# Kernel optimization log

Measured on AMD Instinct MI355X. Metric: run time of the kernel, lower is better.

Reference implementation:

```python
import jax, jax.numpy as jnp
import numpy as np

N_WIRES = 8
DIM = 2 ** N_WIRES  # 256


def _rx(theta):
    # theta: [] or [N] -> [2,2] or [N,2,2] complex64
    c = jnp.cos(theta / 2)
    s = jnp.sin(theta / 2)
    return jnp.stack([jnp.stack([c + 0j, -1j * s], -1),
                      jnp.stack([-1j * s, c + 0j], -1)], -2)


def _ry(theta):
    c = jnp.cos(theta / 2)
    s = jnp.sin(theta / 2)
    return jnp.stack([jnp.stack([c + 0j, -s + 0j], -1),
                      jnp.stack([s + 0j, c + 0j], -1)], -2)


def _rz(theta):
    e = jnp.exp(-1j * theta / 2)
    z = jnp.zeros_like(e)
    return jnp.stack([jnp.stack([e, z], -1),
                      jnp.stack([z, jnp.conj(e)], -1)], -2)


def _apply_1q(state, U, wire):
    # state: [N, DIM]; U: [2,2] (shared) or [N,2,2] (per-sample)
    s = state.reshape(-1, 2 ** wire, 2, 2 ** (N_WIRES - 1 - wire))
    if U.ndim == 2:
        s = jnp.einsum('ab,nxby->nxay', U, s)
    else:
        s = jnp.einsum('nab,nxby->nxay', U, s)
    return s.reshape(-1, DIM)


def _cnot(state, c, t):
    # wire 0 = most significant bit (PennyLane convention)
    s = state.reshape((-1,) + (2,) * N_WIRES)
    ax_c = 1 + c
    s0 = jnp.take(s, 0, axis=ax_c)
    s1 = jnp.take(s, 1, axis=ax_c)
    ax_t = 1 + t if t < c else t  # target axis after control axis removed
    s1 = jnp.flip(s1, axis=ax_t)
    s = jnp.stack([s0, s1], axis=ax_c)
    return s.reshape(-1, DIM)


def _z_signs():
    idx = np.arange(DIM)
    bits = (idx[:, None] >> (N_WIRES - 1 - np.arange(N_WIRES))[None, :]) & 1
    return jnp.asarray(1.0 - 2.0 * bits, dtype=jnp.float32)  # [DIM, 8]


def _circuit(x_flat, params):
    # x_flat: [N, 8] angles; params: [8, 3]
    n = x_flat.shape[0]
    state = jnp.zeros((n, DIM), dtype=jnp.complex64).at[:, 0].set(1.0)
    for i in range(N_WIRES):
        state = _apply_1q(state, _rx(x_flat[:, i]), i)
    for i in range(N_WIRES):
        state = _apply_1q(state, _ry(params[i, 0]), i)
        state = _apply_1q(state, _rz(params[i, 1]), i)
        state = _apply_1q(state, _rx(params[i, 2]), i)
    for i in range(N_WIRES - 1):
        state = _cnot(state, i, i + 1)
    state = _cnot(state, N_WIRES - 1, 0)
    probs = state.real ** 2 + state.imag ** 2  # [N, DIM]
    return probs @ _z_signs()  # [N, 8] PauliZ expvals


def setup_inputs() -> dict:
    key = jax.random.key(0)
    ks = jax.random.split(key, 4)
    B, S = 16, 2048
    embed_dim, ffn_dim = 512, 2048
    return {
        'x': jax.random.normal(ks[0], (B, S, N_WIRES), dtype=jnp.float32),
        'params': jax.random.normal(ks[1], (N_WIRES, 3), dtype=jnp.float32),
        'W1': jax.random.normal(ks[2], (ffn_dim, N_WIRES), dtype=jnp.float32) * 0.1,
        'b1': jnp.zeros((ffn_dim,), dtype=jnp.float32),
        'W2': jax.random.normal(ks[3], (embed_dim, ffn_dim), dtype=jnp.float32) * 0.02,
        'b2': jnp.zeros((embed_dim,), dtype=jnp.float32),
    }


def reference(x, params, W1, b1, W2, b2):
    B, S, _ = x.shape
    ev = _circuit(x.reshape(-1, N_WIRES), params).reshape(B, S, N_WIRES)
    h = jax.nn.relu(ev @ W1.T + b1)
    return h @ W2.T + b2
```

## Files before the change

### kernel.cpp

```cpp
#include <hip/hip_runtime.h>
#include <hip/hip_bf16.h>

#define NS 32768
#define EMB 512
#define KDIM 2048
#define BM 256
#define BN 128
#define NITER (KDIM / 32)

typedef float f32x16 __attribute__((ext_vector_type(16)));
typedef __bf16 bf16x8 __attribute__((ext_vector_type(8)));
typedef __bf16 bf16x2 __attribute__((ext_vector_type(2)));
typedef unsigned int u32;
typedef const __attribute__((address_space(1))) u32* gptr_t;
typedef __attribute__((address_space(3))) u32* lptr_t;

__device__ __forceinline__ void gload_lds16(const void* g, void* l) {
    __builtin_amdgcn_global_load_lds((gptr_t)g, (lptr_t)l, 16, 0, 0);
}

__device__ __forceinline__ u32 pkrelu(float lo, float hi) {
    union { bf16x2 h; u32 u; } c;
    c.h[0] = (__bf16)fmaxf(lo, 0.f);
    c.h[1] = (__bf16)fmaxf(hi, 0.f);
    return c.u;
}

__device__ __forceinline__ bf16x8 mk_af(u32 a, u32 b, u32 c, u32 d) {
    union { u32 u[4]; bf16x8 v; } t;
    t.u[0] = a; t.u[1] = b; t.u[2] = c; t.u[3] = d;
    return t.v;
}

__device__ __forceinline__ void h_to_af(const f32x16 h, bf16x8& af0, bf16x8& af1) {
    af0 = mk_af(pkrelu(h[0], h[1]),  pkrelu(h[2], h[3]),
                pkrelu(h[4], h[5]),  pkrelu(h[6], h[7]));
    af1 = mk_af(pkrelu(h[8], h[9]),  pkrelu(h[10], h[11]),
                pkrelu(h[12], h[13]), pkrelu(h[14], h[15]));
}

__global__ __launch_bounds__(256) void k_prep(const float* __restrict__ W2,
                                              const float* __restrict__ W1,
                                              __hip_bfloat16* __restrict__ W2b,
                                              __hip_bfloat16* __restrict__ W1bg) {
    int t = threadIdx.x;
    if (blockIdx.x < 1024) {
        int i = (blockIdx.x * 256 + t) * 4;
        float4 v = *(const float4*)(W2 + i);
        __hip_bfloat16 o[4];
        o[0] = __float2bfloat16(v.x); o[1] = __float2bfloat16(v.y);
        o[2] = __float2bfloat16(v.z); o[3] = __float2bfloat16(v.w);
        *(ulong1*)(W2b + i) = *(ulong1*)o;
    } else {
        int j = (blockIdx.x - 1024) * 1024 + t * 4;
        float4 w = *(const float4*)(W1 + j);
        __hip_bfloat16 p[4];
        p[0] = __float2bfloat16(w.x); p[1] = __float2bfloat16(w.y);
        p[2] = __float2bfloat16(w.z); p[3] = __float2bfloat16(w.w);
        *(ulong1*)(W1bg + j) = *(ulong1*)p;
    }
}

__global__ __launch_bounds__(256, 2) void k_gemm(
        const float* __restrict__ x,
        const float* __restrict__ params,
        const __hip_bfloat16* __restrict__ W1bg,
        const float* __restrict__ b1,
        const __hip_bfloat16* __restrict__ W2b,
        const float* __restrict__ b2,
        float* __restrict__ C) {
    __shared__ __hip_bfloat16 Bs[4][8 * 512];
    __shared__ __hip_bfloat16 W1s[KDIM * 8];
    __shared__ __hip_bfloat16 b1h[KDIM];
    __shared__ __hip_bfloat16 evs[BM * 8];

    int tid = threadIdx.x, wave = tid >> 6, lane = tid & 63;
    int l31 = lane & 31, half = lane >> 5;
    int bx = blockIdx.x, bm = bx >> 2, bn = bx & 3;

    {
        float K1[8], K2[8];
        #pragma unroll
        for (int i = 0; i < 8; i++) {
            float a = params[i*3+0], b = params[i*3+1], g = params[i*3+2];
            float sa, ca, sb, cb, sg, cg;
            __sincosf(a, &sa, &ca);
            __sincosf(b, &sb, &cb);
            __sincosf(g, &sg, &cg);
            K1[i] = sa*sb*sg + ca*cg;
            K2[i] = cb*sg;
        }
        int n = bm * BM + tid;
        float4 x0 = *(const float4*)(x + (size_t)n*8);
        float4 x1 = *(const float4*)(x + (size_t)n*8 + 4);
        float xs[8] = {x0.x, x0.y, x0.z, x0.w, x1.x, x1.y, x1.z, x1.w};
        float z[8];
        #pragma unroll
        for (int i = 0; i < 8; i++) {
            float s, c;
            __sincosf(xs[i], &s, &c);
            z[i] = c * K1[i] - s * K2[i];
        }
        float evv[8];
        float p = z[0];
        #pragma unroll
        for (int j = 1; j < 8; j++) { p *= z[j]; evv[j] = p; }
        float sfx = z[7];
        #pragma unroll
        for (int j = 6; j >= 1; j--) sfx *= z[j];
        evv[0] = sfx;
        __hip_bfloat16 o[8];
        #pragma unroll
        for (int i = 0; i < 8; i++) o[i] = __float2bfloat16(evv[i]);
        *(bf16x8*)&evs[tid * 8] = *(bf16x8*)o;
    }
    for (int i = tid; i < KDIM; i += 256) {
        int q = (i >> 2) & 3;
        int src = i + ((q == 1) ? 4 : (q == 2) ? -4 : 0);
        *(bf16x8*)&W1s[i * 8] = *(const bf16x8*)(W1bg + (size_t)src * 8);
        b1h[i] = __float2bfloat16(b1[src]);
    }

    const __hip_bfloat16* gBp[2];
    #pragma unroll
    for (int i = 0; i < 2; i++) {
        int f = wave * 2 + i, ni = f >> 1, t = f & 1;
        gBp[i] = W2b + (size_t)(bn*BN + ni*32 + l31) * KDIM + t*16 + half*8;
    }
    #pragma unroll
    for (int b = 0; b < 2; b++) {
        #pragma unroll
        for (int i = 0; i < 2; i++) {
            gload_lds16(gBp[i], &Bs[b][(wave*2 + i) * 512]);
            gBp[i] += 32;
        }
    }

    __syncthreads();

    bf16x8 evB0, evB1;
    if (half == 0) {
        evB0 = *(bf16x8*)&evs[(wave * 64 +      l31) * 8];
        evB1 = *(bf16x8*)&evs[(wave * 64 + 32 + l31) * 8];
    } else {
        evB0 = (bf16x8){};
        evB0[0] = (__bf16)1.0f;
        evB1 = evB0;
    }
    const f32x16 z16 = {};

    f32x16 acc[8] = {};

#define COMPUTE_AF(K0, A00, A01, A10, A11) do {                               \
        bf16x8 w1f;                                                           \
        if (half == 0) {                                                      \
            w1f = *(const bf16x8*)&W1s[((K0) + l31) * 8];                     \
        } else {                                                              \
            w1f = (bf16x8){};                                                 \
            w1f[0] = *(const __bf16*)&b1h[(K0) + l31];                        \
        }                                                                     \
        f32x16 h0 = __builtin_amdgcn_mfma_f32_32x32x16_bf16(w1f, evB0, z16, 0, 0, 0); \
        h_to_af(h0, A00, A01);                                                \
        f32x16 h1 = __builtin_amdgcn_mfma_f32_32x32x16_bf16(w1f, evB1, z16, 0, 0, 0); \
        h_to_af(h1, A10, A11);                                                \
    } while (0)

#define GEMM2_STEP(CB, A00, A01, A10, A11) do {                               \
        __builtin_amdgcn_s_setprio(1);                                        \
        _Pragma("unroll")                                                     \
        for (int ni = 0; ni < 4; ni++) {                                      \
            bf16x8 bf0 = *(bf16x8*)&Bs[CB][(ni*2 + 0) * 512 + lane * 8];      \
            acc[ni]     = __builtin_amdgcn_mfma_f32_32x32x16_bf16(A00, bf0, acc[ni],     0, 0, 0); \
            acc[4 + ni] = __builtin_amdgcn_mfma_f32_32x32x16_bf16(A10, bf0, acc[4 + ni], 0, 0, 0); \
            bf16x8 bf1 = *(bf16x8*)&Bs[CB][(ni*2 + 1) * 512 + lane * 8];      \
            acc[ni]     = __builtin_amdgcn_mfma_f32_32x32x16_bf16(A01, bf1, acc[ni],     0, 0, 0); \
            acc[4 + ni] = __builtin_amdgcn_mfma_f32_32x32x16_bf16(A11, bf1, acc[4 + ni], 0, 0, 0); \
        }                                                                     \
        __builtin_amdgcn_s_setprio(0);                                        \
    } while (0)

#define K_ITER(T, BUF, DO_STAGE, VMC) do {                                    \
        if (DO_STAGE) {                                                       \
            gload_lds16(gBp[0], &Bs[((BUF) + 2) & 3][(wave*2 + 0) * 512]);    \
            gload_lds16(gBp[1], &Bs[((BUF) + 2) & 3][(wave*2 + 1) * 512]);    \
            gBp[0] += 32; gBp[1] += 32;                                       \
        }                                                                     \
        COMPUTE_AF((T) * 32, aA00, aA01, aA10, aA11);                         \
        asm volatile("s_waitcnt vmcnt(" VMC ")" ::: "memory");                \
        __builtin_amdgcn_s_barrier();                                         \
        GEMM2_STEP(BUF, aA00, aA01, aA10, aA11);                              \
    } while (0)

    bf16x8 aA00, aA01, aA10, aA11;

    for (int it0 = 0; it0 < NITER - 4; it0 += 4) {
        K_ITER(it0 + 0, 0, 1, "4");
        K_ITER(it0 + 1, 1, 1, "4");
        K_ITER(it0 + 2, 2, 1, "4");
        K_ITER(it0 + 3, 3, 1, "4");
    }
    K_ITER(NITER - 4, 0, 1, "4");
    K_ITER(NITER - 3, 1, 1, "4");
    K_ITER(NITER - 2, 2, 0, "2");
    K_ITER(NITER - 1, 3, 0, "0");

#undef K_ITER
#undef COMPUTE_AF
#undef GEMM2_STEP

    #pragma unroll
    for (int rg = 0; rg < 2; rg++) {
        int rbase = bm*BM + wave*64 + rg*32 + 4*half;
        #pragma unroll
        for (int ni = 0; ni < 4; ni++) {
            int col = bn*BN + ni*32 + l31;
            float bias = b2[col];
            #pragma unroll
            for (int r = 0; r < 16; r++) {
                int row = rbase + (r & 3) + 8 * (r >> 2);
                C[(size_t)row * EMB + col] = acc[rg*4 + ni][r] + bias;
            }
        }
    }
}

extern "C" void kernel_launch(void* const* d_in, const int* in_sizes, int n_in,
                              void* d_out, int out_size, void* d_ws, size_t ws_size,
                              hipStream_t stream) {
    const float* x      = (const float*)d_in[0];
    const float* params = (const float*)d_in[1];
    const float* W1     = (const float*)d_in[2];
    const float* b1     = (const float*)d_in[3];
    const float* W2     = (const float*)d_in[4];
    const float* b2     = (const float*)d_in[5];
    float* out = (float*)d_out;

    char* ws = (char*)d_ws;
    __hip_bfloat16* W2b  = (__hip_bfloat16*)ws;
    __hip_bfloat16* W1bg = (__hip_bfloat16*)(ws + 2097152);

    k_prep<<<1040, 256, 0, stream>>>(W2, W1, W2b, W1bg);
    k_gemm<<<(NS/BM) * (EMB/BN), 256, 0, stream>>>(x, params, W1bg, b1, W2b, b2, out);
}
```

Baseline: 147.9 us.

## Fuse weight bf16 conversion into GEMM kernel via register-staged W2 loads

Removes the separate prep kernel that converted W2 and W1 to bf16. The GEMM kernel now loads fp32 W2 directly into registers, converts it to bf16 and writes it to LDS with a register-staged software pipeline. This replaces the async global-to-LDS loads. It saves one kernel launch and the intermediate round trip through global memory, but each block now reads twice the W2 bytes (fp32), and the conversion work is repeated by every block that shares the same W2 columns. The pipeline also changes from a 2-deep LDS prefetch to a 1-deep register prefetch, which may expose more load latency.

```diff
diff --git a/kernel.cpp b/kernel.cpp
--- a/kernel.cpp
+++ b/kernel.cpp
@@ -12,11 +12,12 @@
 typedef __bf16 bf16x8 __attribute__((ext_vector_type(8)));
 typedef __bf16 bf16x2 __attribute__((ext_vector_type(2)));
 typedef unsigned int u32;
-typedef const __attribute__((address_space(1))) u32* gptr_t;
-typedef __attribute__((address_space(3))) u32* lptr_t;
-
-__device__ __forceinline__ void gload_lds16(const void* g, void* l) {
-    __builtin_amdgcn_global_load_lds((gptr_t)g, (lptr_t)l, 16, 0, 0);
+
+__device__ __forceinline__ u32 pk2(float lo, float hi) {
+    union { bf16x2 h; u32 u; } c;
+    c.h[0] = (__bf16)lo;
+    c.h[1] = (__bf16)hi;
+    return c.u;
 }
 
 __device__ __forceinline__ u32 pkrelu(float lo, float hi) {
@@ -39,40 +40,18 @@
                 pkrelu(h[12], h[13]), pkrelu(h[14], h[15]));
 }
 
-__global__ __launch_bounds__(256) void k_prep(const float* __restrict__ W2,
-                                              const float* __restrict__ W1,
-                                              __hip_bfloat16* __restrict__ W2b,
-                                              __hip_bfloat16* __restrict__ W1bg) {
-    int t = threadIdx.x;
-    if (blockIdx.x < 1024) {
-        int i = (blockIdx.x * 256 + t) * 4;
-        float4 v = *(const float4*)(W2 + i);
-        __hip_bfloat16 o[4];
-        o[0] = __float2bfloat16(v.x); o[1] = __float2bfloat16(v.y);
-        o[2] = __float2bfloat16(v.z); o[3] = __float2bfloat16(v.w);
-        *(ulong1*)(W2b + i) = *(ulong1*)o;
-    } else {
-        int j = (blockIdx.x - 1024) * 1024 + t * 4;
-        float4 w = *(const float4*)(W1 + j);
-        __hip_bfloat16 p[4];
-        p[0] = __float2bfloat16(w.x); p[1] = __float2bfloat16(w.y);
-        p[2] = __float2bfloat16(w.z); p[3] = __float2bfloat16(w.w);
-        *(ulong1*)(W1bg + j) = *(ulong1*)p;
-    }
-}
-
 __global__ __launch_bounds__(256, 2) void k_gemm(
         const float* __restrict__ x,
         const float* __restrict__ params,
-        const __hip_bfloat16* __restrict__ W1bg,
+        const float* __restrict__ W1,
         const float* __restrict__ b1,
-        const __hip_bfloat16* __restrict__ W2b,
+        const float* __restrict__ W2,
         const float* __restrict__ b2,
         float* __restrict__ C) {
-    __shared__ __hip_bfloat16 Bs[4][8 * 512];
-    __shared__ __hip_bfloat16 W1s[KDIM * 8];
-    __shared__ __hip_bfloat16 b1h[KDIM];
-    __shared__ __hip_bfloat16 evs[BM * 8];
+    __shared__ __align__(16) __hip_bfloat16 Bs[4][8 * 512];
+    __shared__ __align__(16) __hip_bfloat16 W1s[KDIM * 8];
+    __shared__ __align__(16) __hip_bfloat16 b1h[KDIM];
+    __shared__ __align__(16) __hip_bfloat16 evs[BM * 8];
 
     int tid = threadIdx.x, wave = tid >> 6, lane = tid & 63;
     int l31 = lane & 31, half = lane >> 5;
@@ -117,25 +96,44 @@
     for (int i = tid; i < KDIM; i += 256) {
         int q = (i >> 2) & 3;
         int src = i + ((q == 1) ? 4 : (q == 2) ? -4 : 0);
-        *(bf16x8*)&W1s[i * 8] = *(const bf16x8*)(W1bg + (size_t)src * 8);
+        float4 wa = *(const float4*)(W1 + (size_t)src * 8);
+        float4 wb = *(const float4*)(W1 + (size_t)src * 8 + 4);
+        union { u32 u[4]; bf16x8 v; } cw;
+        cw.u[0] = pk2(wa.x, wa.y); cw.u[1] = pk2(wa.z, wa.w);
+        cw.u[2] = pk2(wb.x, wb.y); cw.u[3] = pk2(wb.z, wb.w);
+        *(bf16x8*)&W1s[i * 8] = cw.v;
         b1h[i] = __float2bfloat16(b1[src]);
     }
 
-    const __hip_bfloat16* gBp[2];
-    #pragma unroll
-    for (int i = 0; i < 2; i++) {
-        int f = wave * 2 + i, ni = f >> 1, t = f & 1;
-        gBp[i] = W2b + (size_t)(bn*BN + ni*32 + l31) * KDIM + t*16 + half*8;
-    }
-    #pragma unroll
-    for (int b = 0; b < 2; b++) {
-        #pragma unroll
-        for (int i = 0; i < 2; i++) {
-            gload_lds16(gBp[i], &Bs[b][(wave*2 + i) * 512]);
-            gBp[i] += 32;
-        }
-    }
-
+    const float* gW0;
+    const float* gW1;
+    {
+        int f0 = wave * 2 + 0, f1 = wave * 2 + 1;
+        gW0 = W2 + (size_t)(bn*BN + (f0 >> 1)*32 + l31) * KDIM + (f0 & 1)*16 + half*8;
+        gW1 = W2 + (size_t)(bn*BN + (f1 >> 1)*32 + l31) * KDIM + (f1 & 1)*16 + half*8;
+    }
+    float4 rA0, rA1, rB0, rB1;
+
+#define LOADW2() do {                                                         \
+        rA0 = *(const float4*)gW0; rA1 = *(const float4*)(gW0 + 4);           \
+        rB0 = *(const float4*)gW1; rB1 = *(const float4*)(gW1 + 4);           \
+        gW0 += 32; gW1 += 32;                                                 \
+    } while (0)
+
+#define CVTWRITE(BUFIDX) do {                                                 \
+        union { u32 u[4]; bf16x8 v; } c0, c1;                                 \
+        c0.u[0] = pk2(rA0.x, rA0.y); c0.u[1] = pk2(rA0.z, rA0.w);             \
+        c0.u[2] = pk2(rA1.x, rA1.y); c0.u[3] = pk2(rA1.z, rA1.w);             \
+        c1.u[0] = pk2(rB0.x, rB0.y); c1.u[1] = pk2(rB0.z, rB0.w);             \
+        c1.u[2] = pk2(rB1.x, rB1.y); c1.u[3] = pk2(rB1.z, rB1.w);             \
+        *(bf16x8*)&Bs[BUFIDX][(wave*2 + 0) * 512 + lane * 8] = c0.v;          \
+        *(bf16x8*)&Bs[BUFIDX][(wave*2 + 1) * 512 + lane * 8] = c1.v;          \
+    } while (0)
+
+    LOADW2();
+    asm volatile("s_waitcnt vmcnt(0)" ::: "memory");
+    CVTWRITE(0);
+    LOADW2();
     __syncthreads();
 
     bf16x8 evB0, evB1;
@@ -179,34 +177,35 @@
         __builtin_amdgcn_s_setprio(0);                                        \
     } while (0)
 
-#define K_ITER(T, BUF, DO_STAGE, VMC) do {                                    \
-        if (DO_STAGE) {                                                       \
-            gload_lds16(gBp[0], &Bs[((BUF) + 2) & 3][(wave*2 + 0) * 512]);    \
-            gload_lds16(gBp[1], &Bs[((BUF) + 2) & 3][(wave*2 + 1) * 512]);    \
-            gBp[0] += 32; gBp[1] += 32;                                       \
+#define K_ITER(T, BUF, DO_CVT, DO_ISSUE) do {                                 \
+        COMPUTE_AF((T) * 32, aA00, aA01, aA10, aA11);                         \
+        if (DO_CVT)   CVTWRITE(((BUF) + 1) & 3);                              \
+        if (DO_ISSUE) LOADW2();                                               \
+        if (DO_CVT) {                                                         \
+            asm volatile("s_waitcnt lgkmcnt(0)" ::: "memory");                \
+            __builtin_amdgcn_s_barrier();                                     \
         }                                                                     \
-        COMPUTE_AF((T) * 32, aA00, aA01, aA10, aA11);                         \
-        asm volatile("s_waitcnt vmcnt(" VMC ")" ::: "memory");                \
-        __builtin_amdgcn_s_barrier();                                         \
         GEMM2_STEP(BUF, aA00, aA01, aA10, aA11);                              \
     } while (0)
 
     bf16x8 aA00, aA01, aA10, aA11;
 
     for (int it0 = 0; it0 < NITER - 4; it0 += 4) {
-        K_ITER(it0 + 0, 0, 1, "4");
-        K_ITER(it0 + 1, 1, 1, "4");
-        K_ITER(it0 + 2, 2, 1, "4");
-        K_ITER(it0 + 3, 3, 1, "4");
-    }
-    K_ITER(NITER - 4, 0, 1, "4");
-    K_ITER(NITER - 3, 1, 1, "4");
-    K_ITER(NITER - 2, 2, 0, "2");
-    K_ITER(NITER - 1, 3, 0, "0");
+        K_ITER(it0 + 0, 0, 1, 1);
+        K_ITER(it0 + 1, 1, 1, 1);
+        K_ITER(it0 + 2, 2, 1, 1);
+        K_ITER(it0 + 3, 3, 1, 1);
+    }
+    K_ITER(NITER - 4, 0, 1, 1);
+    K_ITER(NITER - 3, 1, 1, 1);
+    K_ITER(NITER - 2, 2, 1, 0);
+    K_ITER(NITER - 1, 3, 0, 0);
 
 #undef K_ITER
 #undef COMPUTE_AF
 #undef GEMM2_STEP
+#undef CVTWRITE
+#undef LOADW2
 
     #pragma unroll
     for (int rg = 0; rg < 2; rg++) {
@@ -235,10 +234,5 @@
     const float* b2     = (const float*)d_in[5];
     float* out = (float*)d_out;
 
-    char* ws = (char*)d_ws;
-    __hip_bfloat16* W2b  = (__hip_bfloat16*)ws;
-    __hip_bfloat16* W1bg = (__hip_bfloat16*)(ws + 2097152);
-
-    k_prep<<<1040, 256, 0, stream>>>(W2, W1, W2b, W1bg);
-    k_gemm<<<(NS/BM) * (EMB/BN), 256, 0, stream>>>(x, params, W1bg, b1, W2b, b2, out);
-}
+    k_gemm<<<(NS/BM) * (EMB/BN), 256, 0, stream>>>(x, params, W1, b1, W2, b2, out);
+}
```

After: 155.8 us. 5.4% more time.

## Process two K-steps per barrier with paired LDS staging in GEMM2 loop

Applied to the files above, without the earlier changes.

Replaces the per-K-step barrier and staged prefetch with a paired iteration. Each pair computes activation fragments for two K-steps, waits once for all outstanding loads and barriers once, then issues the loads for the next two LDS buffers before running both MFMA steps. This halves the number of barriers and waitcnt points, and gives the scheduler more independent MFMA work between syncs. In exchange it waits on vmcnt(0), which shortens the effective prefetch distance, and adds a second set of A-fragment registers.

```diff
diff --git a/kernel.cpp b/kernel.cpp
--- a/kernel.cpp
+++ b/kernel.cpp
@@ -179,32 +179,34 @@
         __builtin_amdgcn_s_setprio(0);                                        \
     } while (0)
 
-#define K_ITER(T, BUF, DO_STAGE, VMC) do {                                    \
+#define PAIR_ITER(T, BA, BB, DO_STAGE) do {                                   \
+        COMPUTE_AF((T) * 32, aA00, aA01, aA10, aA11);                         \
+        asm volatile("s_waitcnt vmcnt(0)" ::: "memory");                      \
+        __builtin_amdgcn_s_barrier();                                         \
         if (DO_STAGE) {                                                       \
-            gload_lds16(gBp[0], &Bs[((BUF) + 2) & 3][(wave*2 + 0) * 512]);    \
-            gload_lds16(gBp[1], &Bs[((BUF) + 2) & 3][(wave*2 + 1) * 512]);    \
+            gload_lds16(gBp[0], &Bs[((BA)+2)&3][(wave*2 + 0) * 512]);         \
+            gload_lds16(gBp[1], &Bs[((BA)+2)&3][(wave*2 + 1) * 512]);         \
+            gBp[0] += 32; gBp[1] += 32;                                       \
+            gload_lds16(gBp[0], &Bs[((BB)+2)&3][(wave*2 + 0) * 512]);         \
+            gload_lds16(gBp[1], &Bs[((BB)+2)&3][(wave*2 + 1) * 512]);         \
             gBp[0] += 32; gBp[1] += 32;                                       \
         }                                                                     \
-        COMPUTE_AF((T) * 32, aA00, aA01, aA10, aA11);                         \
-        asm volatile("s_waitcnt vmcnt(" VMC ")" ::: "memory");                \
-        __builtin_amdgcn_s_barrier();                                         \
-        GEMM2_STEP(BUF, aA00, aA01, aA10, aA11);                              \
+        GEMM2_STEP(BA, aA00, aA01, aA10, aA11);                               \
+        COMPUTE_AF(((T) + 1) * 32, aB00, aB01, aB10, aB11);                   \
+        GEMM2_STEP(BB, aB00, aB01, aB10, aB11);                               \
     } while (0)
 
     bf16x8 aA00, aA01, aA10, aA11;
-
-    for (int it0 = 0; it0 < NITER - 4; it0 += 4) {
-        K_ITER(it0 + 0, 0, 1, "4");
-        K_ITER(it0 + 1, 1, 1, "4");
-        K_ITER(it0 + 2, 2, 1, "4");
-        K_ITER(it0 + 3, 3, 1, "4");
-    }
-    K_ITER(NITER - 4, 0, 1, "4");
-    K_ITER(NITER - 3, 1, 1, "4");
-    K_ITER(NITER - 2, 2, 0, "2");
-    K_ITER(NITER - 1, 3, 0, "0");
-
-#undef K_ITER
+    bf16x8 aB00, aB01, aB10, aB11;
+
+    for (int p = 0; p < 30; p += 2) {
+        PAIR_ITER(2*p,     0, 1, 1);
+        PAIR_ITER(2*p + 2, 2, 3, 1);
+    }
+    PAIR_ITER(60, 0, 1, 1);
+    PAIR_ITER(62, 2, 3, 0);
+
+#undef PAIR_ITER
 #undef COMPUTE_AF
 #undef GEMM2_STEP
 
```

Result: no change. 150.7 us (+1.9%).

## Widen GEMM block to 512 threads with 2x4 wave grid and deeper prefetch

Applied to the files above, without the earlier changes.

The fused kernel moves from 256-thread blocks covering 256x128 output tiles to 512-thread blocks covering 256x256 tiles. The 8 waves form a 4x2 grid and share the staged W2 tiles and the per-block setup (encoder expectation values, W1/b1 staging). The W2 prefetch depth grows from 2 to 3 buffers. The per-phase schedule is also reordered: the first-half B fragments are loaded early, the code waits on lgkmcnt with a sched_barrier, and a trailing barrier is added each phase. The goal is fewer redundant setup passes and more latency hiding, at the cost of a larger LDS footprint (which likely caps residency at one block per CU) and an extra barrier per K step.

```diff
diff --git a/kernel.cpp b/kernel.cpp
--- a/kernel.cpp
+++ b/kernel.cpp
@@ -5,8 +5,8 @@
 #define EMB 512
 #define KDIM 2048
 #define BM 256
-#define BN 128
-#define NITER (KDIM / 32)
+#define BN 256
+#define NPHASE (KDIM / 32)
 
 typedef float f32x16 __attribute__((ext_vector_type(16)));
 typedef __bf16 bf16x8 __attribute__((ext_vector_type(8)));
@@ -61,7 +61,7 @@
     }
 }
 
-__global__ __launch_bounds__(256, 2) void k_gemm(
+__global__ __launch_bounds__(512, 2) void k_gemm(
         const float* __restrict__ x,
         const float* __restrict__ params,
         const __hip_bfloat16* __restrict__ W1bg,
@@ -69,16 +69,17 @@
         const __hip_bfloat16* __restrict__ W2b,
         const float* __restrict__ b2,
         float* __restrict__ C) {
-    __shared__ __hip_bfloat16 Bs[4][8 * 512];
+    __shared__ __hip_bfloat16 Bs[4][16 * 512];
     __shared__ __hip_bfloat16 W1s[KDIM * 8];
     __shared__ __hip_bfloat16 b1h[KDIM];
     __shared__ __hip_bfloat16 evs[BM * 8];
 
     int tid = threadIdx.x, wave = tid >> 6, lane = tid & 63;
     int l31 = lane & 31, half = lane >> 5;
-    int bx = blockIdx.x, bm = bx >> 2, bn = bx & 3;
-
-    {
+    int wm = wave >> 1, wn = wave & 1;
+    int bx = blockIdx.x, bm = bx >> 1, bn = bx & 1;
+
+    if (tid < 256) {
         float K1[8], K2[8];
         #pragma unroll
         for (int i = 0; i < 8; i++) {
@@ -114,106 +115,110 @@
         for (int i = 0; i < 8; i++) o[i] = __float2bfloat16(evv[i]);
         *(bf16x8*)&evs[tid * 8] = *(bf16x8*)o;
     }
-    for (int i = tid; i < KDIM; i += 256) {
+    for (int i = tid; i < KDIM; i += 512) {
         int q = (i >> 2) & 3;
         int src = i + ((q == 1) ? 4 : (q == 2) ? -4 : 0);
         *(bf16x8*)&W1s[i * 8] = *(const bf16x8*)(W1bg + (size_t)src * 8);
         b1h[i] = __float2bfloat16(b1[src]);
     }
 
-    const __hip_bfloat16* gBp[2];
+    const __hip_bfloat16* gBp0;
+    const __hip_bfloat16* gBp1;
+    {
+        int f0 = wave * 2, f1 = wave * 2 + 1;
+        int r0 = bn*BN + (f0 >> 3)*128 + ((f0 >> 1) & 3)*32 + l31;
+        int r1 = bn*BN + (f1 >> 3)*128 + ((f1 >> 1) & 3)*32 + l31;
+        gBp0 = W2b + (size_t)r0 * KDIM + (f0 & 1)*16 + half*8;
+        gBp1 = W2b + (size_t)r1 * KDIM + (f1 & 1)*16 + half*8;
+    }
     #pragma unroll
-    for (int i = 0; i < 2; i++) {
-        int f = wave * 2 + i, ni = f >> 1, t = f & 1;
-        gBp[i] = W2b + (size_t)(bn*BN + ni*32 + l31) * KDIM + t*16 + half*8;
-    }
-    #pragma unroll
-    for (int b = 0; b < 2; b++) {
-        #pragma unroll
-        for (int i = 0; i < 2; i++) {
-            gload_lds16(gBp[i], &Bs[b][(wave*2 + i) * 512]);
-            gBp[i] += 32;
-        }
-    }
-
+    for (int c = 0; c < 3; c++) {
+        gload_lds16(gBp0, &Bs[c][(wave*2 + 0) * 512]); gBp0 += 32;
+        gload_lds16(gBp1, &Bs[c][(wave*2 + 1) * 512]); gBp1 += 32;
+    }
     __syncthreads();
 
     bf16x8 evB0, evB1;
     if (half == 0) {
-        evB0 = *(bf16x8*)&evs[(wave * 64 +      l31) * 8];
-        evB1 = *(bf16x8*)&evs[(wave * 64 + 32 + l31) * 8];
+        evB0 = *(bf16x8*)&evs[(wm * 64 +      l31) * 8];
+        evB1 = *(bf16x8*)&evs[(wm * 64 + 32 + l31) * 8];
     } else {
         evB0 = (bf16x8){};
         evB0[0] = (__bf16)1.0f;
         evB1 = evB0;
     }
     const f32x16 z16 = {};
+    const int fbase = wn * 8;
 
     f32x16 acc[8] = {};
 
-#define COMPUTE_AF(K0, A00, A01, A10, A11) do {                               \
+#define K_PHASE(T, BUF, DO_STAGE, VMC) do {                                   \
+        const int k0 = (T) * 32;                                              \
+          \
+        bf16x8 bf0[4];                                                        \
+        _Pragma("unroll")                                                     \
+        for (int ni = 0; ni < 4; ni++)                                        \
+            bf0[ni] = *(bf16x8*)&Bs[BUF][(fbase + ni*2 + 0) * 512 + lane * 8];\
         bf16x8 w1f;                                                           \
         if (half == 0) {                                                      \
-            w1f = *(const bf16x8*)&W1s[((K0) + l31) * 8];                     \
+            w1f = *(const bf16x8*)&W1s[(k0 + l31) * 8];                       \
         } else {                                                              \
             w1f = (bf16x8){};                                                 \
-            w1f[0] = *(const __bf16*)&b1h[(K0) + l31];                        \
-        }                                                                     \
-        f32x16 h0 = __builtin_amdgcn_mfma_f32_32x32x16_bf16(w1f, evB0, z16, 0, 0, 0); \
-        h_to_af(h0, A00, A01);                                                \
-        f32x16 h1 = __builtin_amdgcn_mfma_f32_32x32x16_bf16(w1f, evB1, z16, 0, 0, 0); \
-        h_to_af(h1, A10, A11);                                                \
-    } while (0)
-
-#define GEMM2_STEP(CB, A00, A01, A10, A11) do {                               \
-        __builtin_amdgcn_s_setprio(1);                                        \
-        _Pragma("unroll")                                                     \
-        for (int ni = 0; ni < 4; ni++) {                                      \
-            bf16x8 bf0 = *(bf16x8*)&Bs[CB][(ni*2 + 0) * 512 + lane * 8];      \
-            acc[ni]     = __builtin_amdgcn_mfma_f32_32x32x16_bf16(A00, bf0, acc[ni],     0, 0, 0); \
-            acc[4 + ni] = __builtin_amdgcn_mfma_f32_32x32x16_bf16(A10, bf0, acc[4 + ni], 0, 0, 0); \
-            bf16x8 bf1 = *(bf16x8*)&Bs[CB][(ni*2 + 1) * 512 + lane * 8];      \
-            acc[ni]     = __builtin_amdgcn_mfma_f32_32x32x16_bf16(A01, bf1, acc[ni],     0, 0, 0); \
-            acc[4 + ni] = __builtin_amdgcn_mfma_f32_32x32x16_bf16(A11, bf1, acc[4 + ni], 0, 0, 0); \
-        }                                                                     \
-        __builtin_amdgcn_s_setprio(0);                                        \
-    } while (0)
-
-#define K_ITER(T, BUF, DO_STAGE, VMC) do {                                    \
+            w1f[0] = *(const __bf16*)&b1h[k0 + l31];                          \
+        }                                                                     \
         if (DO_STAGE) {                                                       \
-            gload_lds16(gBp[0], &Bs[((BUF) + 2) & 3][(wave*2 + 0) * 512]);    \
-            gload_lds16(gBp[1], &Bs[((BUF) + 2) & 3][(wave*2 + 1) * 512]);    \
-            gBp[0] += 32; gBp[1] += 32;                                       \
-        }                                                                     \
-        COMPUTE_AF((T) * 32, aA00, aA01, aA10, aA11);                         \
+            gload_lds16(gBp0, &Bs[((BUF) + 3) & 3][(wave*2 + 0) * 512]);      \
+            gload_lds16(gBp1, &Bs[((BUF) + 3) & 3][(wave*2 + 1) * 512]);      \
+            gBp0 += 32; gBp1 += 32;                                           \
+        }                                                                     \
         asm volatile("s_waitcnt vmcnt(" VMC ")" ::: "memory");                \
         __builtin_amdgcn_s_barrier();                                         \
-        GEMM2_STEP(BUF, aA00, aA01, aA10, aA11);                              \
+        asm volatile("s_waitcnt lgkmcnt(0)" ::: "memory");                    \
+        __builtin_amdgcn_sched_barrier(0);                                    \
+        __builtin_amdgcn_s_setprio(1);                                        \
+        f32x16 h0 = __builtin_amdgcn_mfma_f32_32x32x16_bf16(w1f, evB0, z16, 0, 0, 0); \
+        f32x16 h1 = __builtin_amdgcn_mfma_f32_32x32x16_bf16(w1f, evB1, z16, 0, 0, 0); \
+        bf16x8 af00, af01, af10, af11;                                        \
+        h_to_af(h0, af00, af01);                                              \
+        h_to_af(h1, af10, af11);                                              \
+                    \
+        bf16x8 bf1[4];                                                        \
+        _Pragma("unroll")                                                     \
+        for (int ni = 0; ni < 4; ni++)                                        \
+            bf1[ni] = *(bf16x8*)&Bs[BUF][(fbase + ni*2 + 1) * 512 + lane * 8];\
+        _Pragma("unroll")                                                     \
+        for (int ni = 0; ni < 4; ni++) {                                      \
+            acc[ni]     = __builtin_amdgcn_mfma_f32_32x32x16_bf16(af00, bf0[ni], acc[ni],     0, 0, 0); \
+            acc[4 + ni] = __builtin_amdgcn_mfma_f32_32x32x16_bf16(af10, bf0[ni], acc[4 + ni], 0, 0, 0); \
+        }                                                                     \
+        _Pragma("unroll")                                                     \
+        for (int ni = 0; ni < 4; ni++) {                                      \
+            acc[ni]     = __builtin_amdgcn_mfma_f32_32x32x16_bf16(af01, bf1[ni], acc[ni],     0, 0, 0); \
+            acc[4 + ni] = __builtin_amdgcn_mfma_f32_32x32x16_bf16(af11, bf1[ni], acc[4 + ni], 0, 0, 0); \
+        }                                                                     \
+        __builtin_amdgcn_s_setprio(0);                                        \
+        __builtin_amdgcn_s_barrier();                                         \
     } while (0)
 
-    bf16x8 aA00, aA01, aA10, aA11;
-
-    for (int it0 = 0; it0 < NITER - 4; it0 += 4) {
-        K_ITER(it0 + 0, 0, 1, "4");
-        K_ITER(it0 + 1, 1, 1, "4");
-        K_ITER(it0 + 2, 2, 1, "4");
-        K_ITER(it0 + 3, 3, 1, "4");
-    }
-    K_ITER(NITER - 4, 0, 1, "4");
-    K_ITER(NITER - 3, 1, 1, "4");
-    K_ITER(NITER - 2, 2, 0, "2");
-    K_ITER(NITER - 1, 3, 0, "0");
-
-#undef K_ITER
-#undef COMPUTE_AF
-#undef GEMM2_STEP
+    for (int it0 = 0; it0 < NPHASE - 4; it0 += 4) {
+        K_PHASE(it0 + 0, 0, 1, "4");
+        K_PHASE(it0 + 1, 1, 1, "4");
+        K_PHASE(it0 + 2, 2, 1, "4");
+        K_PHASE(it0 + 3, 3, 1, "4");
+    }
+    K_PHASE(NPHASE - 4, 0, 1, "4");
+    K_PHASE(NPHASE - 3, 1, 0, "2");
+    K_PHASE(NPHASE - 2, 2, 0, "0");
+    K_PHASE(NPHASE - 1, 3, 0, "0");
+
+#undef K_PHASE
 
     #pragma unroll
     for (int rg = 0; rg < 2; rg++) {
-        int rbase = bm*BM + wave*64 + rg*32 + 4*half;
+        int rbase = bm*BM + wm*64 + rg*32 + 4*half;
         #pragma unroll
         for (int ni = 0; ni < 4; ni++) {
-            int col = bn*BN + ni*32 + l31;
+            int col = bn*BN + wn*128 + ni*32 + l31;
             float bias = b2[col];
             #pragma unroll
             for (int r = 0; r < 16; r++) {
@@ -240,5 +245,5 @@
     __hip_bfloat16* W1bg = (__hip_bfloat16*)(ws + 2097152);
 
     k_prep<<<1040, 256, 0, stream>>>(W2, W1, W2b, W1bg);
-    k_gemm<<<(NS/BM) * (EMB/BN), 256, 0, stream>>>(x, params, W1bg, b1, W2b, b2, out);
-}
+    k_gemm<<<(NS/BM) * (EMB/BN), 512, 0, stream>>>(x, params, W1bg, b1, W2b, b2, out);
+}
```

Result: slower. 151.5 us (+2.4%).
